# Optimization experiments

Measured on AMD Instinct MI355X. Metric: run time of the kernel, lower is better.

Reference implementation:

```python
import jax, jax.numpy as jnp
import numpy as np

T, D, H, AE, DFF, B = 128, 256, 8, 32, 512, 256
EPS = 1e-5


def _xavier(key, shape):
    fan_in, fan_out = shape[-2], shape[-1]
    limit = float(np.sqrt(6.0 / (fan_in + fan_out)))
    return jax.random.uniform(key, shape, jnp.float32, -limit, limit)


def setup_inputs() -> dict:
    key = jax.random.key(0)
    ks = jax.random.split(key, 9)
    return {
        "X": jax.random.normal(ks[0], (B, T, D), jnp.float32),
        "Q": _xavier(ks[1], (T, D, H * AE)),
        "K": _xavier(ks[2], (T, D, H * AE)),
        "V": _xavier(ks[3], (T, D, H * D)),
        "O": _xavier(ks[4], (T, H * D, D)),
        "W_gate": _xavier(ks[5], (T, D, DFF)),
        "W_up": _xavier(ks[6], (T, D, DFF)),
        "W_down": _xavier(ks[7], (T, DFF, D)),
        "gamma1": jnp.ones((D,), jnp.float32),
        "beta1": jnp.zeros((D,), jnp.float32),
        "gamma2": jnp.ones((D,), jnp.float32),
        "beta2": jnp.zeros((D,), jnp.float32),
    }


def _layer_norm(x, gamma, beta):
    mu = jnp.mean(x, axis=-1, keepdims=True)
    var = jnp.mean((x - mu) ** 2, axis=-1, keepdims=True)
    return (x - mu) * jax.lax.rsqrt(var + EPS) * gamma + beta


def reference(X, Q, K, V, O, W_gate, W_up, W_down, gamma1, beta1, gamma2, beta2):
    b, t, d = X.shape
    # --- heterogeneous self-attention (dropout is identity in eval mode) ---
    q = jnp.einsum('btd,tde->bte', X, Q).reshape(b, t, H, AE)
    k = jnp.einsum('btd,tde->bte', X, K).reshape(b, t, H, AE)
    v = jnp.einsum('btd,tdn->btn', X, V).reshape(b, t, H, d)
    scores = jnp.einsum('bthe,bshe->bhts', q, k) / jnp.sqrt(jnp.float32(AE))
    attn = jax.nn.softmax(scores, axis=-1)
    out = jnp.einsum('bhts,bshd->bthd', attn, v).reshape(b, t, H * d)
    attn_out = jnp.einsum('btn,tnd->btd', out, O)
    x = _layer_norm(X + attn_out, gamma1, beta1)
    # --- token-specific SwishGLU FFN ---
    gate = jnp.einsum('btd,tdf->btf', x, W_gate)
    up = jnp.einsum('btd,tdf->btf', x, W_up)
    hidden = jax.nn.silu(gate) * up
    ffn_out = jnp.einsum('btf,tfd->btd', hidden, W_down)
    return _layer_norm(x + ffn_out, gamma2, beta2)
```

## Files before the change

### kernel.cpp

```cpp
#include <hip/hip_runtime.h>
#include <stdint.h>

#define DEVI static __device__ __forceinline__

typedef __attribute__((ext_vector_type(4))) float f32x4;
typedef __attribute__((ext_vector_type(8))) short bf8;
typedef __attribute__((ext_vector_type(4))) unsigned short u16x4;
typedef __attribute__((ext_vector_type(4))) unsigned int u32x4;

DEVI unsigned short f2bf(float f) {
  unsigned u = __builtin_bit_cast(unsigned, f);
  u = (u + 0x7FFFu + ((u >> 16) & 1u)) >> 16;
  return (unsigned short)u;
}
DEVI float bf2f(unsigned short s) {
  return __builtin_bit_cast(float, ((unsigned)s) << 16);
}
DEVI unsigned cvt_pk_bf16(float lo, float hi) {
  unsigned r;
  asm("v_cvt_pk_bf16_f32 %0, %1, %2" : "=v"(r) : "v"(lo), "v"(hi));
  return r;
}
DEVI int swz(int row) { return (((row >> 2) ^ row) & 7) << 4; }
DEVI int swz32(int row) { return (((row >> 1) ^ row) & 3) << 4; }

DEVI void gload16(const void* g, void* l) {
  __builtin_amdgcn_global_load_lds(
      (const __attribute__((address_space(1))) unsigned*)g,
      (__attribute__((address_space(3))) unsigned*)l, 16, 0, 0);
}

template<bool OUT_BF16, int MI, bool SILU>
__global__ __launch_bounds__(512, 4)
void gemm_tk(const unsigned short* __restrict__ A, const float* __restrict__ W0,
             const float* __restrict__ W1, void* __restrict__ C,
             int Ka, int N, int lognx, int logmx, int ldC)
{
  const int j = blockIdx.x;
  const int t = (j & 7) + 8 * (j >> (3 + lognx + logmx));
  const int nblk = (j >> 3) & ((1 << lognx) - 1);
  const int mblk = (j >> (3 + lognx)) & ((1 << logmx) - 1);
  const int n0blk = nblk * 128;
  const float* Wsel = (n0blk >= N) ? W1 : W0;
  const int n0w = (n0blk >= N) ? (n0blk - N) : n0blk;

  const int tid = threadIdx.x;
  const int lane = tid & 63;
  const int wv = tid >> 6;
  const int wrow = wv * (MI * 16);

  __shared__ short As[2][MI * 128 * 32];
  __shared__ short Ws[2][128 * 32];

  f32x4 acc[MI][8];
#pragma unroll
  for (int i = 0; i < MI; ++i)
#pragma unroll
    for (int jj = 0; jj < 8; ++jj) acc[i][jj] = f32x4{0.f, 0.f, 0.f, 0.f};

  const long ldA = 128L * Ka;
  const unsigned short* Ab = A + (long)t * Ka + (long)mblk * 128 * ldA;
  const float* Wb = Wsel + (long)t * Ka * N + n0w;

  const int n0 = (tid & 31) * 4;
  const int kp = tid >> 5;

  auto wload = [&](int kt, f32x4& wlo, f32x4& whi) {
    const float* Wn = Wb + (long)kt * 32 * N;
    wlo = *(const f32x4*)(Wn + (long)(kp * 2) * N + n0);
    whi = *(const f32x4*)(Wn + (long)(kp * 2 + 1) * N + n0);
  };
  auto wcvt = [&](short* buf, const f32x4& wlo, const f32x4& whi) {
#pragma unroll
    for (int jj = 0; jj < 4; ++jj) {
      int n = n0 + jj;
      *(unsigned*)((char*)buf + n * 64 + ((kp * 4) ^ swz32(n))) =
          cvt_pk_bf16(wlo[jj], whi[jj]);
    }
  };
  auto astage = [&](int kt, short* buf) {
#pragma unroll
    for (int it = 0; it < MI; ++it) {
      int ci = tid + it * 512;
      int m = ci >> 2, cb = (ci & 3) * 16;
      gload16((const char*)(Ab + (long)kt * 32 + (long)m * ldA) + (cb ^ swz32(m)),
              (char*)buf + ci * 16);
    }
  };
  const unsigned short* gub = A + ((long)mblk * 128 * 128 + t) * 1024;
  auto aload_silu = [&](int kt, bf8& g8, bf8& u8) {
    const int m = tid >> 2, cb8 = (tid & 3) * 8;
    const long base = (long)m * 131072 + kt * 32 + cb8;
    g8 = *(const bf8*)(gub + base);
    u8 = *(const bf8*)(gub + base + 512);
  };
  auto awrite_silu = [&](short* buf, const bf8& g8, const bf8& u8) {
    const int m = tid >> 2, cbB = (tid & 3) * 16;
    float h[8];
#pragma unroll
    for (int jj = 0; jj < 8; ++jj) {
      float gg = bf2f((unsigned short)g8[jj]);
      float uu = bf2f((unsigned short)u8[jj]);
      h[jj] = gg / (1.f + __expf(-gg)) * uu;
    }
    u32x4 w;
#pragma unroll
    for (int p = 0; p < 4; ++p) w[p] = cvt_pk_bf16(h[2 * p], h[2 * p + 1]);
    *(u32x4*)((char*)buf + m * 64 + (cbB ^ swz32(m))) = w;
  };
  auto mfma_tile = [&](const short* abuf, const short* wbuf) {
    const int kb2 = (lane >> 4) * 16;
    bf8 a[MI];
#pragma unroll
    for (int mi = 0; mi < MI; ++mi) {
      const int m0 = wrow + mi * 16 + (lane & 15);
      a[mi] = *(const bf8*)((const char*)abuf + m0 * 64 + (kb2 ^ swz32(m0)));
    }
#pragma unroll
    for (int ni = 0; ni < 8; ++ni) {
      const int n = ni * 16 + (lane & 15);
      bf8 bfr = *(const bf8*)((const char*)wbuf + n * 64 + (kb2 ^ swz32(n)));
#pragma unroll
      for (int mi = 0; mi < MI; ++mi)
        acc[mi][ni] = __builtin_amdgcn_mfma_f32_16x16x32_bf16(a[mi], bfr, acc[mi][ni], 0, 0, 0);
    }
  };

  const int nt = Ka >> 5;

  f32x4 wloA, whiA, wloB, whiB;
  if constexpr (SILU) {
    bf8 g0, u0;
    aload_silu(0, g0, u0);
    awrite_silu(&As[0][0], g0, u0);
  } else {
    astage(0, &As[0][0]);
  }
  wload(0, wloA, whiA);
  wload(1, wloB, whiB);
  wcvt(&Ws[0][0], wloA, whiA);

  for (int kt = 0; kt < nt; kt += 2) {
    __syncthreads();
    bf8 gE, uE;
    if (kt + 2 < nt) wload(kt + 2, wloA, whiA);
    if (kt + 1 < nt) {
      if constexpr (SILU) aload_silu(kt + 1, gE, uE);
      else astage(kt + 1, &As[1][0]);
    }
    mfma_tile(&As[0][0], &Ws[0][0]);
    wcvt(&Ws[1][0], wloB, whiB);
    if constexpr (SILU) { if (kt + 1 < nt) awrite_silu(&As[1][0], gE, uE); }

    __syncthreads();
    bf8 gO, uO;
    if (kt + 3 < nt) wload(kt + 3, wloB, whiB);
    if (kt + 2 < nt) {
      if constexpr (SILU) aload_silu(kt + 2, gO, uO);
      else astage(kt + 2, &As[0][0]);
    }
    mfma_tile(&As[1][0], &Ws[1][0]);
    if (kt + 2 < nt) wcvt(&Ws[0][0], wloA, whiA);
    if constexpr (SILU) { if (kt + 2 < nt) awrite_silu(&As[0][0], gO, uO); }
  }

#pragma unroll
  for (int mi = 0; mi < MI; ++mi)
#pragma unroll
    for (int ni = 0; ni < 8; ++ni)
#pragma unroll
      for (int r = 0; r < 4; ++r) {
        int m = mblk * 128 + wrow + mi * 16 + (lane >> 4) * 4 + r;
        int n = n0blk + ni * 16 + (lane & 15);
        long off = ((long)m * 128 + t) * ldC + n;
        float v = acc[mi][ni][r];
        if constexpr (OUT_BF16) reinterpret_cast<unsigned short*>(C)[off] = f2bf(v);
        else reinterpret_cast<float*>(C)[off] = v;
      }
}

__global__ __launch_bounds__(256)
void cvt_bf(const float* __restrict__ in, unsigned short* __restrict__ out, long n)
{
  long i = ((long)blockIdx.x * 256 + threadIdx.x) * 8;
  if (i >= n) return;
  f32x4 a = *reinterpret_cast<const f32x4*>(in + i);
  f32x4 b = *reinterpret_cast<const f32x4*>(in + i + 4);
  u16x4 w0, w1;
#pragma unroll
  for (int j = 0; j < 4; ++j) { w0[j] = f2bf(a[j]); w1[j] = f2bf(b[j]); }
  *reinterpret_cast<u16x4*>(out + i) = w0;
  *reinterpret_cast<u16x4*>(out + i + 4) = w1;
}

DEVI void stage_write_v(short* buf, f32x4 r0, f32x4 r1, int s2, int d0)
{
  const unsigned* a = reinterpret_cast<const unsigned*>(&r0);
  const unsigned* c = reinterpret_cast<const unsigned*>(&r1);
#pragma unroll
  for (int j = 0; j < 8; ++j) {
    unsigned lo = (j & 1) ? (a[j >> 1] >> 16) : (a[j >> 1] & 0xFFFFu);
    unsigned hi = (j & 1) ? (c[j >> 1] >> 16) : (c[j >> 1] & 0xFFFFu);
    int d = d0 + j;
    *reinterpret_cast<unsigned*>(reinterpret_cast<char*>(buf) + d * 64 + ((4 * s2) ^ swz32(d))) =
        lo | (hi << 16);
  }
}

__global__ __launch_bounds__(512, 4)
void attn_k(const unsigned short* __restrict__ qk, const unsigned short* __restrict__ vg,
            unsigned short* __restrict__ cat)
{
  const int h = blockIdx.x, b = blockIdx.y;
  const int tid = threadIdx.x, lane = tid & 63, wv = tid >> 6;
  const int wrow = wv * 16;

  __shared__ short ps[128 * 128];
  __shared__ short vs[2][256 * 32];

  const long qkBase = ((long)b * 128) * 512 + h * 32;
  const long vgBase = ((long)b * 128) * 2048 + h * 256;
  const int kb_ = (lane >> 4) * 8;

  const int s2 = tid & 15;
  const int d0 = (tid >> 4) * 8;

  f32x4 r0, r1;
  {
    const unsigned short* src = vg + vgBase + (long)(2 * s2) * 2048 + d0;
    r0 = *reinterpret_cast<const f32x4*>(src);
    r1 = *reinterpret_cast<const f32x4*>(src + 2048);
  }

  f32x4 sacc[8];
#pragma unroll
  for (int c = 0; c < 8; ++c) sacc[c] = f32x4{0.f, 0.f, 0.f, 0.f};
  bf8 aq;
  {
    int row = wrow + (lane & 15);
    aq = *reinterpret_cast<const bf8*>(qk + qkBase + (long)row * 512 + kb_);
  }
#pragma unroll
  for (int ni = 0; ni < 8; ++ni) {
    int s = ni * 16 + (lane & 15);
    bf8 bk = *reinterpret_cast<const bf8*>(qk + qkBase + 256 + (long)s * 512 + kb_);
    sacc[ni] = __builtin_amdgcn_mfma_f32_16x16x32_bf16(aq, bk, sacc[ni], 0, 0, 0);
  }

  const float scale = 0.17677669529663687f;
  float sinv[4];
#pragma unroll
  for (int r = 0; r < 4; ++r) {
    int row = wrow + (lane >> 4) * 4 + r;
    float vv[8];
    float mx = -1e30f;
#pragma unroll
    for (int c = 0; c < 8; ++c) { vv[c] = sacc[c][r] * scale; mx = fmaxf(mx, vv[c]); }
#pragma unroll
    for (int mm = 1; mm < 16; mm <<= 1) mx = fmaxf(mx, __shfl_xor(mx, mm, 64));
    float s_ = 0.f;
#pragma unroll
    for (int c = 0; c < 8; ++c) { vv[c] = __expf(vv[c] - mx); s_ += vv[c]; }
#pragma unroll
    for (int mm = 1; mm < 16; mm <<= 1) s_ += __shfl_xor(s_, mm, 64);
    sinv[r] = 1.0f / s_;
#pragma unroll
    for (int c = 0; c < 8; ++c) {
      int col = c * 16 + (lane & 15);
      int byte = row * 256 + ((col * 2) ^ swz(row));
      *reinterpret_cast<unsigned short*>(reinterpret_cast<char*>(ps) + byte) = f2bf(vv[c]);
    }
  }

  stage_write_v(&vs[0][0], r0, r1, s2, d0);

  f32x4 oacc[16];
#pragma unroll
  for (int c = 0; c < 16; ++c) oacc[c] = f32x4{0.f, 0.f, 0.f, 0.f};

#pragma unroll 1
  for (int cs = 0; cs < 4; ++cs) {
    __syncthreads();
    if (cs < 3) {
      const unsigned short* src = vg + vgBase + (long)((cs + 1) * 32 + 2 * s2) * 2048 + d0;
      r0 = *reinterpret_cast<const f32x4*>(src);
      r1 = *reinterpret_cast<const f32x4*>(src + 2048);
    }
    const int kglob = cs * 32 + kb_;
    bf8 ap;
    {
      int row = wrow + (lane & 15);
      int byte = row * 256 + ((kglob * 2) ^ swz(row));
      ap = *reinterpret_cast<const bf8*>(reinterpret_cast<const char*>(ps) + byte);
    }
    __builtin_amdgcn_s_setprio(1);
#pragma unroll
    for (int c = 0; c < 16; ++c) {
      int d = c * 16 + (lane & 15);
      bf8 bv = *reinterpret_cast<const bf8*>(
          reinterpret_cast<const char*>(&vs[cs & 1][0]) + d * 64 + ((kb_ * 2) ^ swz32(d)));
      oacc[c] = __builtin_amdgcn_mfma_f32_16x16x32_bf16(ap, bv, oacc[c], 0, 0, 0);
    }
    __builtin_amdgcn_s_setprio(0);
    if (cs < 3) stage_write_v(&vs[(cs + 1) & 1][0], r0, r1, s2, d0);
  }

#pragma unroll
  for (int c = 0; c < 16; ++c)
#pragma unroll
    for (int r = 0; r < 4; ++r) {
      int tt = wrow + (lane >> 4) * 4 + r;
      int d = c * 16 + (lane & 15);
      float v = oacc[c][r] * sinv[r];
      long off = ((long)b * 128 + tt) * 2048 + h * 256 + d;
      cat[off] = f2bf(v);
    }
}

template<bool WF, bool WB>
__global__ __launch_bounds__(256)
void ln_k(const unsigned short* __restrict__ a, const unsigned short* __restrict__ bsrc,
          const float* __restrict__ gamma, const float* __restrict__ beta,
          float* __restrict__ of, unsigned short* __restrict__ ob)
{
  const int row = blockIdx.x * 4 + (threadIdx.x >> 6);
  const int lane = threadIdx.x & 63;
  const long base = (long)row * 256 + lane * 4;
  u16x4 ua = *reinterpret_cast<const u16x4*>(a + base);
  u16x4 ub = *reinterpret_cast<const u16x4*>(bsrc + base);
  f32x4 x;
#pragma unroll
  for (int j = 0; j < 4; ++j) x[j] = bf2f(ua[j]) + bf2f(ub[j]);
  float s = x[0] + x[1] + x[2] + x[3];
  float s2 = x[0] * x[0] + x[1] * x[1] + x[2] * x[2] + x[3] * x[3];
#pragma unroll
  for (int mm = 1; mm < 64; mm <<= 1) { s += __shfl_xor(s, mm, 64); s2 += __shfl_xor(s2, mm, 64); }
  float mean = s * (1.f / 256.f);
  float var = fmaxf(s2 * (1.f / 256.f) - mean * mean, 0.f);
  float inv = rsqrtf(var + 1e-5f);
  f32x4 g = *reinterpret_cast<const f32x4*>(gamma + lane * 4);
  f32x4 be = *reinterpret_cast<const f32x4*>(beta + lane * 4);
  f32x4 y;
#pragma unroll
  for (int j = 0; j < 4; ++j) y[j] = (x[j] - mean) * inv * g[j] + be[j];
  if constexpr (WF) *reinterpret_cast<f32x4*>(of + base) = y;
  if constexpr (WB) {
    u16x4 w;
#pragma unroll
    for (int j = 0; j < 4; ++j) w[j] = f2bf(y[j]);
    *reinterpret_cast<u16x4*>(ob + base) = w;
  }
}

extern "C" void kernel_launch(void* const* d_in, const int* in_sizes, int n_in,
                              void* d_out, int out_size, void* d_ws, size_t ws_size,
                              hipStream_t stream)
{
  const float* X  = (const float*)d_in[0];
  const float* Qw = (const float*)d_in[1];
  const float* Kw = (const float*)d_in[2];
  const float* Vw = (const float*)d_in[3];
  const float* Ow = (const float*)d_in[4];
  const float* Wg = (const float*)d_in[5];
  const float* Wu = (const float*)d_in[6];
  const float* Wd = (const float*)d_in[7];
  const float* g1 = (const float*)d_in[8];
  const float* b1 = (const float*)d_in[9];
  const float* g2 = (const float*)d_in[10];
  const float* b2 = (const float*)d_in[11];

  char* ws = (char*)d_ws;
  const size_t MiB = 1048576;
  unsigned short* Xb  = (unsigned short*)(ws);
  unsigned short* qkb = (unsigned short*)(ws + 16 * MiB);
  char* regA = ws + 48 * MiB;
  char* regB = regA + 128 * MiB;

  unsigned short* vb     = (unsigned short*)regA;
  unsigned short* cat    = (unsigned short*)regB;
  unsigned short* attnpb = (unsigned short*)(regA);
  unsigned short* x1b    = (unsigned short*)(regA + 16 * MiB);
  unsigned short* gateup = (unsigned short*)(regA + 32 * MiB);
  unsigned short* ffnb   = (unsigned short*)(regA + 96 * MiB);
  float* out = (float*)d_out;

  dim3 blk(256), gblk(512);
  cvt_bf<<<dim3(4096), blk, 0, stream>>>(X, Xb, (long)8388608);
  gemm_tk<true, 2, false><<<dim3(512), gblk, 0, stream>>>(Xb, Qw, Kw, (void*)qkb, 256, 256, 2, 0, 512);
  gemm_tk<true, 2, false><<<dim3(2048), gblk, 0, stream>>>(Xb, Vw, Vw, (void*)vb, 256, 2048, 4, 0, 2048);
  attn_k<<<dim3(8, 256), gblk, 0, stream>>>(qkb, vb, cat);
  gemm_tk<true, 1, false><<<dim3(512), gblk, 0, stream>>>(cat, Ow, Ow, (void*)attnpb, 2048, 256, 1, 1, 256);
  ln_k<false, true><<<dim3(8192), blk, 0, stream>>>(Xb, attnpb, g1, b1, (float*)nullptr, x1b);
  gemm_tk<true, 2, false><<<dim3(1024), gblk, 0, stream>>>(x1b, Wg, Wu, (void*)gateup, 256, 512, 3, 0, 1024);
  gemm_tk<true, 1, true><<<dim3(512), gblk, 0, stream>>>(gateup, Wd, Wd, (void*)ffnb, 512, 256, 1, 1, 256);
  ln_k<true, false><<<dim3(8192), blk, 0, stream>>>(x1b, ffnb, g2, b2, out, (unsigned short*)nullptr);
}
```

Measured before the change: 444.5 us.

## Fuse down-projection GEMM with residual add and final LayerNorm

Adds a dedicated down-projection kernel in which each block computes the full 256-wide output row tile, so the residual add and second LayerNorm can be applied in registers. This replaces the separate down-GEMM plus ln_k launch and removes the bf16 ffn intermediate round trip through memory. The cost is that the grid drops to 256 blocks with larger per-block tiles and launch_bounds(512,2), which lowers parallelism and occupancy. The SILU path is also removed from the generic GEMM template.

```diff
diff --git a/kernel.cpp b/kernel.cpp
--- a/kernel.cpp
+++ b/kernel.cpp
@@ -30,7 +30,7 @@
       (__attribute__((address_space(3))) unsigned*)l, 16, 0, 0);
 }
 
-template<bool OUT_BF16, int MI, bool SILU>
+template<bool OUT_BF16, int MI>
 __global__ __launch_bounds__(512, 4)
 void gemm_tk(const unsigned short* __restrict__ A, const float* __restrict__ W0,
              const float* __restrict__ W1, void* __restrict__ C,
@@ -87,27 +87,6 @@
               (char*)buf + ci * 16);
     }
   };
-  const unsigned short* gub = A + ((long)mblk * 128 * 128 + t) * 1024;
-  auto aload_silu = [&](int kt, bf8& g8, bf8& u8) {
-    const int m = tid >> 2, cb8 = (tid & 3) * 8;
-    const long base = (long)m * 131072 + kt * 32 + cb8;
-    g8 = *(const bf8*)(gub + base);
-    u8 = *(const bf8*)(gub + base + 512);
-  };
-  auto awrite_silu = [&](short* buf, const bf8& g8, const bf8& u8) {
-    const int m = tid >> 2, cbB = (tid & 3) * 16;
-    float h[8];
-#pragma unroll
-    for (int jj = 0; jj < 8; ++jj) {
-      float gg = bf2f((unsigned short)g8[jj]);
-      float uu = bf2f((unsigned short)u8[jj]);
-      h[jj] = gg / (1.f + __expf(-gg)) * uu;
-    }
-    u32x4 w;
-#pragma unroll
-    for (int p = 0; p < 4; ++p) w[p] = cvt_pk_bf16(h[2 * p], h[2 * p + 1]);
-    *(u32x4*)((char*)buf + m * 64 + (cbB ^ swz32(m))) = w;
-  };
   auto mfma_tile = [&](const short* abuf, const short* wbuf) {
     const int kb2 = (lane >> 4) * 16;
     bf8 a[MI];
@@ -129,39 +108,23 @@
   const int nt = Ka >> 5;
 
   f32x4 wloA, whiA, wloB, whiB;
-  if constexpr (SILU) {
-    bf8 g0, u0;
-    aload_silu(0, g0, u0);
-    awrite_silu(&As[0][0], g0, u0);
-  } else {
-    astage(0, &As[0][0]);
-  }
+  astage(0, &As[0][0]);
   wload(0, wloA, whiA);
   wload(1, wloB, whiB);
   wcvt(&Ws[0][0], wloA, whiA);
 
   for (int kt = 0; kt < nt; kt += 2) {
     __syncthreads();
-    bf8 gE, uE;
     if (kt + 2 < nt) wload(kt + 2, wloA, whiA);
-    if (kt + 1 < nt) {
-      if constexpr (SILU) aload_silu(kt + 1, gE, uE);
-      else astage(kt + 1, &As[1][0]);
-    }
+    if (kt + 1 < nt) astage(kt + 1, &As[1][0]);
     mfma_tile(&As[0][0], &Ws[0][0]);
     wcvt(&Ws[1][0], wloB, whiB);
-    if constexpr (SILU) { if (kt + 1 < nt) awrite_silu(&As[1][0], gE, uE); }
 
     __syncthreads();
-    bf8 gO, uO;
     if (kt + 3 < nt) wload(kt + 3, wloB, whiB);
-    if (kt + 2 < nt) {
-      if constexpr (SILU) aload_silu(kt + 2, gO, uO);
-      else astage(kt + 2, &As[0][0]);
-    }
+    if (kt + 2 < nt) astage(kt + 2, &As[0][0]);
     mfma_tile(&As[1][0], &Ws[1][0]);
     if (kt + 2 < nt) wcvt(&Ws[0][0], wloA, whiA);
-    if constexpr (SILU) { if (kt + 2 < nt) awrite_silu(&As[0][0], gO, uO); }
   }
 
 #pragma unroll
@@ -177,6 +140,153 @@
         if constexpr (OUT_BF16) reinterpret_cast<unsigned short*>(C)[off] = f2bf(v);
         else reinterpret_cast<float*>(C)[off] = v;
       }
+}
+
+__global__ __launch_bounds__(512, 2)
+void down_ln_k(const unsigned short* __restrict__ gu, const float* __restrict__ Wd,
+               const unsigned short* __restrict__ x1, const float* __restrict__ gamma,
+               const float* __restrict__ beta, float* __restrict__ out)
+{
+  const int j = blockIdx.x;
+  const int t = (j & 7) + 8 * (j >> 4);
+  const int mblk = (j >> 3) & 1;
+
+  const int tid = threadIdx.x;
+  const int lane = tid & 63;
+  const int wv = tid >> 6;
+  const int wrow = wv * 16;
+
+  __shared__ short As[2][128 * 32];
+  __shared__ short Ws[2][256 * 32];
+  __shared__ float gsh[256], bsh[256];
+
+  if (tid < 256) { gsh[tid] = gamma[tid]; bsh[tid] = beta[tid]; }
+
+  f32x4 acc[16];
+#pragma unroll
+  for (int c = 0; c < 16; ++c) acc[c] = f32x4{0.f, 0.f, 0.f, 0.f};
+
+  const unsigned short* gub = gu + ((long)mblk * 128 * 128 + t) * 1024;
+  const float* Wb = Wd + (long)t * 512 * 256;
+
+  const int n0 = (tid & 63) * 4;
+  const int kp = tid >> 6;
+
+  auto wload = [&](int kt, f32x4& l0, f32x4& h0, f32x4& l1, f32x4& h1) {
+    const float* Wn = Wb + (long)kt * 32 * 256;
+    l0 = *(const f32x4*)(Wn + (long)(kp * 2) * 256 + n0);
+    h0 = *(const f32x4*)(Wn + (long)(kp * 2 + 1) * 256 + n0);
+    l1 = *(const f32x4*)(Wn + (long)((kp + 8) * 2) * 256 + n0);
+    h1 = *(const f32x4*)(Wn + (long)((kp + 8) * 2 + 1) * 256 + n0);
+  };
+  auto wcvt = [&](short* buf, const f32x4& l0, const f32x4& h0,
+                  const f32x4& l1, const f32x4& h1) {
+#pragma unroll
+    for (int jj = 0; jj < 4; ++jj) {
+      int n = n0 + jj;
+      *(unsigned*)((char*)buf + n * 64 + ((kp * 4) ^ swz32(n))) =
+          cvt_pk_bf16(l0[jj], h0[jj]);
+      *(unsigned*)((char*)buf + n * 64 + (((kp + 8) * 4) ^ swz32(n))) =
+          cvt_pk_bf16(l1[jj], h1[jj]);
+    }
+  };
+  auto aload_silu = [&](int kt, bf8& g8, bf8& u8) {
+    const int m = tid >> 2, cb8 = (tid & 3) * 8;
+    const long base = (long)m * 131072 + kt * 32 + cb8;
+    g8 = *(const bf8*)(gub + base);
+    u8 = *(const bf8*)(gub + base + 512);
+  };
+  auto awrite_silu = [&](short* buf, const bf8& g8, const bf8& u8) {
+    const int m = tid >> 2, cbB = (tid & 3) * 16;
+    float h[8];
+#pragma unroll
+    for (int jj = 0; jj < 8; ++jj) {
+      float gg = bf2f((unsigned short)g8[jj]);
+      float uu = bf2f((unsigned short)u8[jj]);
+      h[jj] = gg / (1.f + __expf(-gg)) * uu;
+    }
+    u32x4 w;
+#pragma unroll
+    for (int p = 0; p < 4; ++p) w[p] = cvt_pk_bf16(h[2 * p], h[2 * p + 1]);
+    *(u32x4*)((char*)buf + m * 64 + (cbB ^ swz32(m))) = w;
+  };
+  auto mfma_tile = [&](const short* abuf, const short* wbuf) {
+    const int kb2 = (lane >> 4) * 16;
+    const int m0 = wrow + (lane & 15);
+    bf8 a = *(const bf8*)((const char*)abuf + m0 * 64 + (kb2 ^ swz32(m0)));
+#pragma unroll
+    for (int ni = 0; ni < 16; ++ni) {
+      const int n = ni * 16 + (lane & 15);
+      bf8 bfr = *(const bf8*)((const char*)wbuf + n * 64 + (kb2 ^ swz32(n)));
+      acc[ni] = __builtin_amdgcn_mfma_f32_16x16x32_bf16(a, bfr, acc[ni], 0, 0, 0);
+    }
+  };
+
+  {
+    bf8 g0, u0;
+    aload_silu(0, g0, u0);
+    awrite_silu(&As[0][0], g0, u0);
+    f32x4 l0, h0, l1, h1;
+    wload(0, l0, h0, l1, h1);
+    wcvt(&Ws[0][0], l0, h0, l1, h1);
+  }
+  int cur = 0;
+  for (int kt = 0; kt < 16; ++kt) {
+    __syncthreads();
+    bf8 gn, un;
+    f32x4 l0, h0, l1, h1;
+    const bool more = (kt + 1) < 16;
+    if (more) { wload(kt + 1, l0, h0, l1, h1); aload_silu(kt + 1, gn, un); }
+    mfma_tile(&As[cur][0], &Ws[cur][0]);
+    if (more) {
+      wcvt(&Ws[cur ^ 1][0], l0, h0, l1, h1);
+      awrite_silu(&As[cur ^ 1][0], gn, un);
+      cur ^= 1;
+    }
+  }
+
+  const long mg0 = (long)mblk * 128;
+  short* xsh = &Ws[0][0];
+  for (int hh = 0; hh < 2; ++hh) {
+    __syncthreads();
+#pragma unroll
+    for (int it = 0; it < 4; ++it) {
+      int ci = tid + it * 512;
+      int rloc = ci >> 5, c16 = ci & 31;
+      gload16(x1 + ((mg0 + 64 * hh + rloc) * 128 + t) * 256 + c16 * 8,
+              (char*)xsh + ci * 16);
+    }
+    __syncthreads();
+    if ((wv >> 2) == hh) {
+#pragma unroll
+      for (int r = 0; r < 4; ++r) {
+        const int mloc = wrow + (lane >> 4) * 4 + r;
+        const int lrow = mloc & 63;
+        float x[16];
+        float s = 0.f, s2 = 0.f;
+#pragma unroll
+        for (int ni = 0; ni < 16; ++ni) {
+          int n = ni * 16 + (lane & 15);
+          float v = acc[ni][r] + bf2f((unsigned short)xsh[lrow * 256 + n]);
+          x[ni] = v; s += v; s2 += v * v;
+        }
+#pragma unroll
+        for (int mm = 1; mm < 16; mm <<= 1) {
+          s += __shfl_xor(s, mm, 64);
+          s2 += __shfl_xor(s2, mm, 64);
+        }
+        float mean = s * (1.f / 256.f);
+        float var = fmaxf(s2 * (1.f / 256.f) - mean * mean, 0.f);
+        float inv = rsqrtf(var + 1e-5f);
+#pragma unroll
+        for (int ni = 0; ni < 16; ++ni) {
+          int n = ni * 16 + (lane & 15);
+          out[((mg0 + mloc) * 128 + t) * 256 + n] =
+              (x[ni] - mean) * inv * gsh[n] + bsh[n];
+        }
+      }
+    }
+  }
 }
 
 __global__ __launch_bounds__(256)
@@ -381,17 +491,15 @@
   unsigned short* attnpb = (unsigned short*)(regA);
   unsigned short* x1b    = (unsigned short*)(regA + 16 * MiB);
   unsigned short* gateup = (unsigned short*)(regA + 32 * MiB);
-  unsigned short* ffnb   = (unsigned short*)(regA + 96 * MiB);
   float* out = (float*)d_out;
 
   dim3 blk(256), gblk(512);
   cvt_bf<<<dim3(4096), blk, 0, stream>>>(X, Xb, (long)8388608);
-  gemm_tk<true, 2, false><<<dim3(512), gblk, 0, stream>>>(Xb, Qw, Kw, (void*)qkb, 256, 256, 2, 0, 512);
-  gemm_tk<true, 2, false><<<dim3(2048), gblk, 0, stream>>>(Xb, Vw, Vw, (void*)vb, 256, 2048, 4, 0, 2048);
+  gemm_tk<true, 2><<<dim3(512), gblk, 0, stream>>>(Xb, Qw, Kw, (void*)qkb, 256, 256, 2, 0, 512);
+  gemm_tk<true, 2><<<dim3(2048), gblk, 0, stream>>>(Xb, Vw, Vw, (void*)vb, 256, 2048, 4, 0, 2048);
   attn_k<<<dim3(8, 256), gblk, 0, stream>>>(qkb, vb, cat);
-  gemm_tk<true, 1, false><<<dim3(512), gblk, 0, stream>>>(cat, Ow, Ow, (void*)attnpb, 2048, 256, 1, 1, 256);
+  gemm_tk<true, 1><<<dim3(512), gblk, 0, stream>>>(cat, Ow, Ow, (void*)attnpb, 2048, 256, 1, 1, 256);
   ln_k<false, true><<<dim3(8192), blk, 0, stream>>>(Xb, attnpb, g1, b1, (float*)nullptr, x1b);
-  gemm_tk<true, 2, false><<<dim3(1024), gblk, 0, stream>>>(x1b, Wg, Wu, (void*)gateup, 256, 512, 3, 0, 1024);
-  gemm_tk<true, 1, true><<<dim3(512), gblk, 0, stream>>>(gateup, Wd, Wd, (void*)ffnb, 512, 256, 1, 1, 256);
-  ln_k<true, false><<<dim3(8192), blk, 0, stream>>>(x1b, ffnb, g2, b2, out, (unsigned short*)nullptr);
-}
+  gemm_tk<true, 2><<<dim3(1024), gblk, 0, stream>>>(x1b, Wg, Wu, (void*)gateup, 256, 512, 3, 0, 1024);
+  down_ln_k<<<dim3(256), gblk, 0, stream>>>(gateup, Wd, x1b, g2, b2, out);
+}
```

Measured after the change: 451.4 us. No clear change (+1.6%).
